# Kernel optimization log

Measured on AMD Instinct MI355X. Metric: run time of the kernel, lower is better.

Reference implementation:

```python
import jax, jax.numpy as jnp
import numpy as np

N_TOKEN = 1024
FFN_MULT = 4
B = 32
D = 1024
LN_EPS = 1e-5


def _layer_norm(x, gamma, beta):
    mu = jnp.mean(x, axis=-1, keepdims=True)
    var = jnp.var(x, axis=-1, keepdims=True)
    return (x - mu) * jax.lax.rsqrt(var + LN_EPS) * gamma + beta


def setup_inputs() -> dict:
    key = jax.random.key(0)
    ks = jax.random.split(key, 12)
    n, m = N_TOKEN, FFN_MULT * N_TOKEN
    s_in = 1.0 / np.sqrt(n)
    s_ff = 1.0 / np.sqrt(m)
    return {
        "Q": jax.random.normal(ks[0], (B, n), jnp.float32),
        "K": jax.random.normal(ks[1], (B, n, D), jnp.float32),
        "V": jax.random.normal(ks[2], (B, n, D), jnp.float32),
        "mu_w": jax.random.uniform(ks[3], (n, n), jnp.float32, -s_in, s_in),
        "mu_b": jax.random.uniform(ks[4], (n,), jnp.float32, -s_in, s_in),
        "sigma_w": jax.random.uniform(ks[5], (n, n), jnp.float32, -s_in, s_in),
        "sigma_b": jax.random.uniform(ks[6], (n,), jnp.float32, -s_in, s_in),
        "ffn_w1": jax.random.uniform(ks[7], (m, n), jnp.float32, -s_in, s_in),
        "ffn_b1": jax.random.uniform(ks[8], (m,), jnp.float32, -s_in, s_in),
        "ffn_w2": jax.random.uniform(ks[9], (n, m), jnp.float32, -s_ff, s_ff),
        "ffn_b2": jax.random.uniform(ks[10], (n,), jnp.float32, -s_ff, s_ff),
        "ln_ff_g": jnp.ones((n,), jnp.float32),
        "ln_ff_b": jnp.zeros((n,), jnp.float32),
        "ln_q_g": jnp.ones((n,), jnp.float32),
        "ln_q_b": jnp.zeros((n,), jnp.float32),
    }


def reference(Q, K, V, mu_w, mu_b, sigma_w, sigma_b, ffn_w1, ffn_b1,
              ffn_w2, ffn_b2, ln_ff_g, ln_ff_b, ln_q_g, ln_q_b):
    q = _layer_norm(Q, ln_q_g, ln_q_b)                       # (B, n)
    mu = jnp.tanh(q @ mu_w.T + mu_b)[..., None]              # (B, n, 1)
    sigma = (q @ sigma_w.T + sigma_b)[..., None]             # (B, n, 1)
    # Gaussian-kernel pseudo-attention: broadcast over D then reduce
    S = jnp.exp(-0.5 * (K - mu) ** 2 / (sigma ** 2 + 1e-8))  # (B, n, D)
    A = jnp.sum(S * V, axis=-1)                              # (B, n)
    x = A + Q
    h = _layer_norm(x, ln_ff_g, ln_ff_b)
    h = jax.nn.silu(h @ ffn_w1.T + ffn_b1) @ ffn_w2.T + ffn_b2
    return x + h
```

## Files before the change

### kernel.cpp

```cpp
#include <hip/hip_runtime.h>

#define N_TOK  1024
#define D_DIM  1024
#define M_FFN  4096

typedef float f32x4 __attribute__((ext_vector_type(4)));

__device__ __forceinline__ float wave_reduce(float v) {
    #pragma unroll
    for (int off = 32; off > 0; off >>= 1) v += __shfl_xor(v, off);
    return v;
}

__global__ void ln_kernel(const float* __restrict__ X,
                          const float* __restrict__ gam,
                          const float* __restrict__ bet,
                          float* __restrict__ Y) {
    int b = blockIdx.x, t = threadIdx.x;
    float4 x = ((const float4*)(X + (size_t)b * N_TOK))[t];
    float s = x.x + x.y + x.z + x.w;
    float q = x.x*x.x + x.y*x.y + x.z*x.z + x.w*x.w;
    s = wave_reduce(s); q = wave_reduce(q);
    __shared__ float sa[4], sb[4];
    int wid = t >> 6;
    if ((t & 63) == 0) { sa[wid] = s; sb[wid] = q; }
    __syncthreads();
    float ts = sa[0] + sa[1] + sa[2] + sa[3];
    float tq = sb[0] + sb[1] + sb[2] + sb[3];
    float mean = ts * (1.f / N_TOK);
    float var  = tq * (1.f / N_TOK) - mean * mean;
    float rs = rsqrtf(var + 1e-5f);
    float4 g4 = ((const float4*)gam)[t];
    float4 b4 = ((const float4*)bet)[t];
    float4 o;
    o.x = (x.x - mean) * rs * g4.x + b4.x;
    o.y = (x.y - mean) * rs * g4.y + b4.y;
    o.z = (x.z - mean) * rs * g4.z + b4.z;
    o.w = (x.w - mean) * rs * g4.w + b4.w;
    ((float4*)(Y + (size_t)b * N_TOK))[t] = o;
}

__device__ __forceinline__ void gemm_body(const float* __restrict__ A,
                                          const float* __restrict__ W,
                                          float* __restrict__ C,
                                          const float* __restrict__ bias,
                                          int N, int K, int kchunk, int mode,
                                          int bx, int by) {
    int t = threadIdx.x;
    int lane = t & 63, wid = t >> 6;
    int ksub = lane & 15, nsub = lane >> 4;
    int mhalf = wid & 1, ngrp = wid >> 1;
    int n = bx * 8 + ngrp * 4 + nsub;
    int k0 = by * kchunk + ksub * 4;
    const float* wp = W + (size_t)n * K + k0;
    const float* ap = A + (size_t)mhalf * 16 * K + k0;
    float acc[16];
    #pragma unroll
    for (int j = 0; j < 16; j++) acc[j] = 0.f;
    f32x4 w4 = __builtin_nontemporal_load((const f32x4*)wp);
    for (int kk = 0; kk < kchunk; kk += 64) {
        f32x4 wn;
        if (kk + 64 < kchunk)
            wn = __builtin_nontemporal_load((const f32x4*)(wp + kk + 64));
        #pragma unroll
        for (int j = 0; j < 16; j++) {
            float4 a4 = *(const float4*)(ap + (size_t)j * K + kk);
            acc[j] += a4.x*w4.x + a4.y*w4.y + a4.z*w4.z + a4.w*w4.w;
        }
        w4 = wn;
    }
    #pragma unroll
    for (int j = 0; j < 16; j++) {
        #pragma unroll
        for (int off = 1; off < 16; off <<= 1)
            acc[j] += __shfl_xor(acc[j], off);
    }
    if (ksub == 0) {
        int mbase = mhalf * 16;
        if (mode == 2) {
            #pragma unroll
            for (int j = 0; j < 16; j++)
                atomicAdd(C + (size_t)(mbase + j) * N + n, acc[j]);
        } else if (mode == 1) {
            float bn = bias[n];
            #pragma unroll
            for (int j = 0; j < 16; j++) {
                float z = acc[j] + bn;
                C[(size_t)(mbase + j) * N + n] = z / (1.f + __expf(-z));
            }
        } else {
            #pragma unroll
            for (int j = 0; j < 16; j++)
                C[(size_t)(mbase + j) * N + n] = acc[j];
        }
    }
}

__global__ void gemm_mu_sigma(const float* __restrict__ A,
                              const float* __restrict__ W0,
                              const float* __restrict__ W1,
                              float* __restrict__ C0,
                              float* __restrict__ C1) {
    const float* W = blockIdx.z ? W1 : W0;
    float*       C = blockIdx.z ? C1 : C0;
    gemm_body(A, W, C, nullptr, 1024, 1024, 1024, 0, blockIdx.x, 0);
}

__global__ void gemm_ffn1(const float* __restrict__ A,
                          const float* __restrict__ W,
                          float* __restrict__ C,
                          const float* __restrict__ bias) {
    gemm_body(A, W, C, bias, 4096, 1024, 1024, 1, blockIdx.x, 0);
}

__global__ void gemm_ffn2(const float* __restrict__ A,
                          const float* __restrict__ W,
                          float* __restrict__ C) {
    gemm_body(A, W, C, nullptr, 1024, 4096, 2048, 2, blockIdx.x, blockIdx.y);
}

__global__ void attn_kernel(const float* __restrict__ Kp,
                            const float* __restrict__ Vp,
                            const float* __restrict__ Qp,
                            const float* __restrict__ mu_acc,
                            const float* __restrict__ sg_acc,
                            const float* __restrict__ mu_b,
                            const float* __restrict__ sg_b,
                            float* __restrict__ xo) {
    int t = threadIdx.x;
    int lane = t & 63, wid = t >> 6;
    int row = blockIdx.x * 4 + wid;
    const f32x4* kp = (const f32x4*)(Kp + (size_t)row * D_DIM);
    const f32x4* vp = (const f32x4*)(Vp + (size_t)row * D_DIM);
    f32x4 k4[4], v4[4];
    #pragma unroll
    for (int c = 0; c < 4; c++) k4[c] = __builtin_nontemporal_load(kp + c * 64 + lane);
    #pragma unroll
    for (int c = 0; c < 4; c++) v4[c] = __builtin_nontemporal_load(vp + c * 64 + lane);
    int i = row & (N_TOK - 1);
    float mu = tanhf(mu_acc[row] + mu_b[i]);
    float sg = sg_acc[row] + sg_b[i];
    float coef = -0.5f / (sg * sg + 1e-8f);
    float acc = 0.f;
    #pragma unroll
    for (int c = 0; c < 4; c++) {
        float d;
        d = k4[c].x - mu; acc += __expf(coef * d * d) * v4[c].x;
        d = k4[c].y - mu; acc += __expf(coef * d * d) * v4[c].y;
        d = k4[c].z - mu; acc += __expf(coef * d * d) * v4[c].z;
        d = k4[c].w - mu; acc += __expf(coef * d * d) * v4[c].w;
    }
    acc = wave_reduce(acc);
    if (lane == 0) xo[row] = acc + Qp[row];
}

__global__ void final_kernel(const float* __restrict__ x,
                             const float* __restrict__ acc2,
                             const float* __restrict__ b2,
                             float* __restrict__ out) {
    int idx = blockIdx.x * 256 + threadIdx.x;
    out[idx] = x[idx] + acc2[idx] + b2[idx & (N_TOK - 1)];
}

extern "C" void kernel_launch(void* const* d_in, const int* in_sizes, int n_in,
                              void* d_out, int out_size, void* d_ws, size_t ws_size,
                              hipStream_t stream) {
    const float* Q       = (const float*)d_in[0];
    const float* Kp      = (const float*)d_in[1];
    const float* Vp      = (const float*)d_in[2];
    const float* mu_w    = (const float*)d_in[3];
    const float* mu_b    = (const float*)d_in[4];
    const float* sigma_w = (const float*)d_in[5];
    const float* sigma_b = (const float*)d_in[6];
    const float* w1      = (const float*)d_in[7];
    const float* b1      = (const float*)d_in[8];
    const float* w2      = (const float*)d_in[9];
    const float* b2      = (const float*)d_in[10];
    const float* ln_ff_g = (const float*)d_in[11];
    const float* ln_ff_b = (const float*)d_in[12];
    const float* ln_q_g  = (const float*)d_in[13];
    const float* ln_q_b  = (const float*)d_in[14];

    float* mu_acc = (float*)d_ws;
    float* sg_acc = mu_acc + 32768;
    float* f2_acc = sg_acc + 32768;
    float* xbuf   = f2_acc + 32768;
    float* qln    = xbuf   + 32768;
    float* h0     = qln    + 32768;
    float* g      = h0     + 32768;

    hipMemsetAsync(f2_acc, 0, (size_t)32768 * sizeof(float), stream);

    ln_kernel<<<32, 256, 0, stream>>>(Q, ln_q_g, ln_q_b, qln);

    gemm_mu_sigma<<<dim3(128, 1, 2), 256, 0, stream>>>(
        qln, mu_w, sigma_w, mu_acc, sg_acc);

    attn_kernel<<<8192, 256, 0, stream>>>(Kp, Vp, Q, mu_acc, sg_acc,
                                          mu_b, sigma_b, xbuf);

    ln_kernel<<<32, 256, 0, stream>>>(xbuf, ln_ff_b == ln_ff_g ? ln_ff_g : ln_ff_g, ln_ff_b, h0);

    gemm_ffn1<<<512, 256, 0, stream>>>(h0, w1, g, b1);

    gemm_ffn2<<<dim3(128, 2), 256, 0, stream>>>(g, w2, f2_acc);
    final_kernel<<<128, 256, 0, stream>>>(xbuf, f2_acc, b2, (float*)d_out);
}
```

Before: 428.6 us.

## Split-K mu/sigma and FFN2 GEMMs, two rows per wave in attention, drop W prefetch

The mu/sigma GEMM now splits K into two chunks and accumulates with atomics, and FFN2 splits K four ways instead of two, so more blocks run in parallel. The memset is widened to zero all the accumulators. The attention kernel processes two rows per wave, giving each lane more independent loads in flight. The software prefetch of weights in the GEMM inner loop is removed. Together these add atomic traffic and give up the explicit weight prefetch.

```diff
diff --git a/kernel.cpp b/kernel.cpp
--- a/kernel.cpp
+++ b/kernel.cpp
@@ -57,17 +57,13 @@
     float acc[16];
     #pragma unroll
     for (int j = 0; j < 16; j++) acc[j] = 0.f;
-    f32x4 w4 = __builtin_nontemporal_load((const f32x4*)wp);
     for (int kk = 0; kk < kchunk; kk += 64) {
-        f32x4 wn;
-        if (kk + 64 < kchunk)
-            wn = __builtin_nontemporal_load((const f32x4*)(wp + kk + 64));
+        f32x4 w4 = __builtin_nontemporal_load((const f32x4*)(wp + kk));
         #pragma unroll
         for (int j = 0; j < 16; j++) {
             float4 a4 = *(const float4*)(ap + (size_t)j * K + kk);
             acc[j] += a4.x*w4.x + a4.y*w4.y + a4.z*w4.z + a4.w*w4.w;
         }
-        w4 = wn;
     }
     #pragma unroll
     for (int j = 0; j < 16; j++) {
@@ -103,7 +99,7 @@
                               float* __restrict__ C1) {
     const float* W = blockIdx.z ? W1 : W0;
     float*       C = blockIdx.z ? C1 : C0;
-    gemm_body(A, W, C, nullptr, 1024, 1024, 1024, 0, blockIdx.x, 0);
+    gemm_body(A, W, C, nullptr, 1024, 1024, 512, 2, blockIdx.x, blockIdx.y);
 }
 
 __global__ void gemm_ffn1(const float* __restrict__ A,
@@ -116,7 +112,7 @@
 __global__ void gemm_ffn2(const float* __restrict__ A,
                           const float* __restrict__ W,
                           float* __restrict__ C) {
-    gemm_body(A, W, C, nullptr, 1024, 4096, 2048, 2, blockIdx.x, blockIdx.y);
+    gemm_body(A, W, C, nullptr, 1024, 4096, 1024, 2, blockIdx.x, blockIdx.y);
 }
 
 __global__ void attn_kernel(const float* __restrict__ Kp,
@@ -129,29 +125,46 @@
                             float* __restrict__ xo) {
     int t = threadIdx.x;
     int lane = t & 63, wid = t >> 6;
-    int row = blockIdx.x * 4 + wid;
-    const f32x4* kp = (const f32x4*)(Kp + (size_t)row * D_DIM);
-    const f32x4* vp = (const f32x4*)(Vp + (size_t)row * D_DIM);
-    f32x4 k4[4], v4[4];
-    #pragma unroll
-    for (int c = 0; c < 4; c++) k4[c] = __builtin_nontemporal_load(kp + c * 64 + lane);
-    #pragma unroll
-    for (int c = 0; c < 4; c++) v4[c] = __builtin_nontemporal_load(vp + c * 64 + lane);
-    int i = row & (N_TOK - 1);
-    float mu = tanhf(mu_acc[row] + mu_b[i]);
-    float sg = sg_acc[row] + sg_b[i];
-    float coef = -0.5f / (sg * sg + 1e-8f);
-    float acc = 0.f;
+    int row0 = blockIdx.x * 8 + wid * 2;
+    int row1 = row0 + 1;
+    const f32x4* kp0 = (const f32x4*)(Kp + (size_t)row0 * D_DIM);
+    const f32x4* vp0 = (const f32x4*)(Vp + (size_t)row0 * D_DIM);
+    const f32x4* kp1 = (const f32x4*)(Kp + (size_t)row1 * D_DIM);
+    const f32x4* vp1 = (const f32x4*)(Vp + (size_t)row1 * D_DIM);
+    f32x4 ka[4], va[4], kb[4], vb[4];
+    #pragma unroll
+    for (int c = 0; c < 4; c++) ka[c] = __builtin_nontemporal_load(kp0 + c * 64 + lane);
+    #pragma unroll
+    for (int c = 0; c < 4; c++) kb[c] = __builtin_nontemporal_load(kp1 + c * 64 + lane);
+    #pragma unroll
+    for (int c = 0; c < 4; c++) va[c] = __builtin_nontemporal_load(vp0 + c * 64 + lane);
+    #pragma unroll
+    for (int c = 0; c < 4; c++) vb[c] = __builtin_nontemporal_load(vp1 + c * 64 + lane);
+    int i0 = row0 & (N_TOK - 1), i1 = row1 & (N_TOK - 1);
+    float mu0 = tanhf(mu_acc[row0] + mu_b[i0]);
+    float mu1 = tanhf(mu_acc[row1] + mu_b[i1]);
+    float sg0 = sg_acc[row0] + sg_b[i0];
+    float sg1 = sg_acc[row1] + sg_b[i1];
+    float c0 = -0.5f / (sg0 * sg0 + 1e-8f);
+    float c1 = -0.5f / (sg1 * sg1 + 1e-8f);
+    float acc0 = 0.f, acc1 = 0.f, d;
     #pragma unroll
     for (int c = 0; c < 4; c++) {
-        float d;
-        d = k4[c].x - mu; acc += __expf(coef * d * d) * v4[c].x;
-        d = k4[c].y - mu; acc += __expf(coef * d * d) * v4[c].y;
-        d = k4[c].z - mu; acc += __expf(coef * d * d) * v4[c].z;
-        d = k4[c].w - mu; acc += __expf(coef * d * d) * v4[c].w;
-    }
-    acc = wave_reduce(acc);
-    if (lane == 0) xo[row] = acc + Qp[row];
+        d = ka[c].x - mu0; acc0 += __expf(c0 * d * d) * va[c].x;
+        d = ka[c].y - mu0; acc0 += __expf(c0 * d * d) * va[c].y;
+        d = ka[c].z - mu0; acc0 += __expf(c0 * d * d) * va[c].z;
+        d = ka[c].w - mu0; acc0 += __expf(c0 * d * d) * va[c].w;
+        d = kb[c].x - mu1; acc1 += __expf(c1 * d * d) * vb[c].x;
+        d = kb[c].y - mu1; acc1 += __expf(c1 * d * d) * vb[c].y;
+        d = kb[c].z - mu1; acc1 += __expf(c1 * d * d) * vb[c].z;
+        d = kb[c].w - mu1; acc1 += __expf(c1 * d * d) * vb[c].w;
+    }
+    acc0 = wave_reduce(acc0);
+    acc1 = wave_reduce(acc1);
+    if (lane == 0) {
+        xo[row0] = acc0 + Qp[row0];
+        xo[row1] = acc1 + Qp[row1];
+    }
 }
 
 __global__ void final_kernel(const float* __restrict__ x,
@@ -189,20 +202,20 @@
     float* h0     = qln    + 32768;
     float* g      = h0     + 32768;
 
-    hipMemsetAsync(f2_acc, 0, (size_t)32768 * sizeof(float), stream);
+    hipMemsetAsync(mu_acc, 0, (size_t)98304 * sizeof(float), stream);
 
     ln_kernel<<<32, 256, 0, stream>>>(Q, ln_q_g, ln_q_b, qln);
 
-    gemm_mu_sigma<<<dim3(128, 1, 2), 256, 0, stream>>>(
+    gemm_mu_sigma<<<dim3(128, 2, 2), 256, 0, stream>>>(
         qln, mu_w, sigma_w, mu_acc, sg_acc);
 
-    attn_kernel<<<8192, 256, 0, stream>>>(Kp, Vp, Q, mu_acc, sg_acc,
+    attn_kernel<<<4096, 256, 0, stream>>>(Kp, Vp, Q, mu_acc, sg_acc,
                                           mu_b, sigma_b, xbuf);
 
-    ln_kernel<<<32, 256, 0, stream>>>(xbuf, ln_ff_b == ln_ff_g ? ln_ff_g : ln_ff_g, ln_ff_b, h0);
+    ln_kernel<<<32, 256, 0, stream>>>(xbuf, ln_ff_g, ln_ff_b, h0);
 
     gemm_ffn1<<<512, 256, 0, stream>>>(h0, w1, g, b1);
 
-    gemm_ffn2<<<dim3(128, 2), 256, 0, stream>>>(g, w2, f2_acc);
+    gemm_ffn2<<<dim3(128, 4), 256, 0, stream>>>(g, w2, f2_acc);
     final_kernel<<<128, 256, 0, stream>>>(xbuf, f2_acc, b2, (float*)d_out);
 }
```

After: 372.8 us. 13.0% less time.
